# Kernel tuning notes

Measured on AMD Instinct MI355X. Metric: run time of the kernel, lower is better.

The kernel has to match this reference:

```python
import jax, jax.numpy as jnp
import numpy as np

B, S, D, H = 2, 2048, 2048, 16
HD = D // H  # 128
ROPE_BASE = 10000.0


def _rope_tables(seq_len, head_dim, dtype=jnp.float32):
    inv_freq = 1.0 / (ROPE_BASE ** (jnp.arange(0, head_dim, 2, dtype=jnp.float32) / head_dim))
    t = jnp.arange(seq_len, dtype=jnp.float32)
    freqs = jnp.outer(t, inv_freq)  # [S, HD/2]
    # broadcast shape [1, S, 1, HD/2]
    return jnp.cos(freqs)[None, :, None, :].astype(dtype), jnp.sin(freqs)[None, :, None, :].astype(dtype)


def _apply_rope(x, cos, sin):
    # x: [B, S, H, HD]; interleaved split, output concatenated by halves (matches torch code)
    x1 = x[..., ::2]
    x2 = x[..., 1::2]
    return jnp.concatenate([x1 * cos - x2 * sin, x1 * sin + x2 * cos], axis=-1)


def setup_inputs() -> dict:
    key = jax.random.key(0)
    ks = jax.random.split(key, 9)
    xavier = lambda k: jax.random.uniform(k, (D, D), jnp.float32, -1.0, 1.0) * np.sqrt(6.0 / (D + D))
    return {
        "x": jax.random.normal(ks[0], (B, S, D), jnp.float32),
        "attention_mask": jnp.ones((B, S), jnp.int32),
        "wq": xavier(ks[1]), "bq": jnp.zeros((D,), jnp.float32),
        "wk": xavier(ks[2]), "bk": jnp.zeros((D,), jnp.float32),
        "wv": xavier(ks[3]), "bv": jnp.zeros((D,), jnp.float32),
        "wo": xavier(ks[4]), "bo": jnp.zeros((D,), jnp.float32),
    }


def reference(x, attention_mask, wq, bq, wk, bk, wv, bv, wo, bo):
    b, s, _ = x.shape
    scale = HD ** -0.5
    q = (x @ wq + bq).reshape(b, s, H, HD)
    k = (x @ wk + bk).reshape(b, s, H, HD)
    v = (x @ wv + bv).reshape(b, s, H, HD)
    cos, sin = _rope_tables(s, HD, x.dtype)
    q = _apply_rope(q, cos, sin)
    k = _apply_rope(k, cos, sin)
    # [B, H, S, S]
    scores = jnp.einsum('bqhd,bkhd->bhqk', q, k) * scale
    mask = attention_mask[:, None, None, :]  # 2D mask -> [B,1,1,S]
    scores = jnp.where(mask == 0, jnp.asarray(-1e9, scores.dtype), scores)
    attn = jax.nn.softmax(scores, axis=-1)
    out = jnp.einsum('bhqk,bkhd->bqhd', attn, v).reshape(b, s, D)
    return out @ wo + bo
```

## Files before the change

kernel.cpp:

```cpp
#include <hip/hip_runtime.h>

#define Bc 2
#define Sc 2048
#define Dc 2048
#define Hc 16
#define HDc 128
#define Mc 4096

typedef __bf16 bf16_t;
typedef __bf16 bf16x4 __attribute__((ext_vector_type(4)));
typedef __bf16 bf16x8 __attribute__((ext_vector_type(8)));
typedef float f32x4 __attribute__((ext_vector_type(4)));
typedef float f32x16 __attribute__((ext_vector_type(16)));

__device__ __forceinline__ f32x4 mfma16(bf16x8 a, bf16x8 b, f32x4 c) {
  return __builtin_amdgcn_mfma_f32_16x16x32_bf16(a, b, c, 0, 0, 0);
}
__device__ __forceinline__ f32x16 mfma32(bf16x8 a, bf16x8 b, f32x16 c) {
  return __builtin_amdgcn_mfma_f32_32x32x16_bf16(a, b, c, 0, 0, 0);
}

typedef const unsigned __attribute__((address_space(1))) gu32_t;
typedef unsigned __attribute__((address_space(3))) lu32_t;

__device__ __forceinline__ void gload_lds16(const void* g, void* l) {
  gu32_t* gp = (gu32_t*)(unsigned long long)g;
  lu32_t* lp = (lu32_t*)(unsigned)(unsigned long long)l;
  __builtin_amdgcn_global_load_lds(gp, lp, 16, 0, 0);
}

__device__ __forceinline__ unsigned cvtpk(float lo, float hi_) {
  unsigned r;
  asm("v_cvt_pk_bf16_f32 %0, %1, %2" : "=v"(r) : "v"(lo), "v"(hi_));
  return r;
}
__device__ __forceinline__ void plswap(unsigned& a, unsigned& b) {
  asm volatile("v_permlane32_swap_b32 %0, %1" : "+v"(a), "+v"(b));
}

__global__ void cvt_bf16_kernel(const float* __restrict__ in, bf16_t* __restrict__ out, int n4) {
  int i = blockIdx.x * blockDim.x + threadIdx.x;
  if (i < n4) {
    float4 v = ((const float4*)in)[i];
    bf16x4 o;
    o[0] = (bf16_t)v.x; o[1] = (bf16_t)v.y; o[2] = (bf16_t)v.z; o[3] = (bf16_t)v.w;
    ((bf16x4*)out)[i] = o;
  }
}

__global__ void transpose_cvt_kernel(const float* __restrict__ w, bf16_t* __restrict__ wt) {
  __shared__ float tile[32][33];
  const int tx = threadIdx.x, ty = threadIdx.y;
  const int n0 = blockIdx.x * 32, k0 = blockIdx.y * 32;
#pragma unroll
  for (int i = 0; i < 32; i += 8)
    tile[ty + i][tx] = w[(size_t)(k0 + ty + i) * Dc + n0 + tx];
  __syncthreads();
#pragma unroll
  for (int i = 0; i < 32; i += 8)
    wt[(size_t)(n0 + ty + i) * Dc + k0 + tx] = (bf16_t)tile[tx][ty + i];
}

template <int MODE, int NT>
__global__ __launch_bounds__(512, 1) void gemm3_kernel(
    const bf16_t* __restrict__ A, const bf16_t* __restrict__ Bt,
    const float* __restrict__ bias0, const float* __restrict__ bias1,
    const float* __restrict__ bias2,
    void* __restrict__ out0, void* __restrict__ out1, void* __restrict__ out2) {
  __shared__ __align__(16) bf16_t sA[3][128 * 64];
  __shared__ __align__(16) bf16_t sB[3][256 * 64];
  const int tid = threadIdx.x;
  const int lane = tid & 63, wid = tid >> 6;
  const int l15 = lane & 15, g = lane >> 4;
  const int sw = l15 & 7;
  const int wrow = wid >> 2, wcol = wid & 3;

  const int nwg = 32 * NT, cpx = nwg / 8;
  const int wgid = ((int)blockIdx.x & 7) * cpx + ((int)blockIdx.x >> 3);
  const int mt = wgid & 31, nt = wgid >> 5;
  const int m0 = mt * 128, n0 = nt * 256;

  const bf16_t* Ab = A + (size_t)m0 * 2048;
  const bf16_t* Bb = Bt + (size_t)n0 * 2048;

#define G3_STAGE(kt)                                                          \
  {                                                                           \
    const int sl_ = (kt) % 3;                                                 \
    const int kc_ = (kt) * 64;                                                \
    _Pragma("unroll") for (int i_ = 0; i_ < 2; ++i_) {                        \
      int s_ = i_ * 512 + tid;                                                \
      int r_ = s_ >> 3;                                                       \
      int c_ = ((s_ & 7) ^ (r_ & 7)) * 8;                                     \
      gload_lds16(Ab + (size_t)r_ * 2048 + kc_ + c_,                          \
                  (char*)&sA[sl_][0] + s_ * 16);                              \
    }                                                                         \
    _Pragma("unroll") for (int i_ = 0; i_ < 4; ++i_) {                        \
      int s_ = i_ * 512 + tid;                                                \
      int r_ = s_ >> 3;                                                       \
      int c_ = ((s_ & 7) ^ (r_ & 7)) * 8;                                     \
      gload_lds16(Bb + (size_t)r_ * 2048 + kc_ + c_,                          \
                  (char*)&sB[sl_][0] + s_ * 16);                              \
    }                                                                         \
  }

  f32x4 acc[4][4] = {};

  G3_STAGE(0);
  G3_STAGE(1);

#define G3_RD(co)                                                                   \
  _Pragma("unroll") for (int mi = 0; mi < 4; ++mi)                                  \
      afrag[mi] = *(const bf16x8*)(pA + (wrow * 64 + mi * 16 + l15) * 128 + (co));  \
  _Pragma("unroll") for (int ni = 0; ni < 4; ++ni)                                  \
      bfrag[ni] = *(const bf16x8*)(pB + (wcol * 64 + ni * 16 + l15) * 128 + (co));

#define G3_MM                                                                 \
  __builtin_amdgcn_s_setprio(1);                                              \
  _Pragma("unroll") for (int mi = 0; mi < 4; ++mi)                            \
      _Pragma("unroll") for (int ni = 0; ni < 4; ++ni)                        \
          acc[mi][ni] = mfma16(afrag[mi], bfrag[ni], acc[mi][ni]);            \
  __builtin_amdgcn_s_setprio(0);

#define G3_BODY(t, DOSTG, VMSTR)                                              \
  {                                                                           \
    asm volatile("s_waitcnt vmcnt(" VMSTR ")" ::: "memory");                  \
    __builtin_amdgcn_s_barrier();                                             \
    __builtin_amdgcn_sched_barrier(0);                                        \
    const int sl = (t) % 3;                                                   \
    const char* pA = (const char*)&sA[sl][0];                                 \
    const char* pB = (const char*)&sB[sl][0];                                 \
    bf16x8 afrag[4], bfrag[4];                                                \
    G3_RD((g ^ sw) * 16);                                                     \
    if (DOSTG) G3_STAGE((t) + 2);                                             \
    G3_MM;                                                                    \
    G3_RD(((4 + g) ^ sw) * 16);                                               \
    G3_MM;                                                                    \
  }

  for (int t = 0; t < 30; ++t) G3_BODY(t, 1, "6");
  G3_BODY(30, 0, "6");
  G3_BODY(31, 0, "0");

#undef G3_BODY
#undef G3_MM
#undef G3_RD
#undef G3_STAGE

#pragma unroll
  for (int mi = 0; mi < 4; ++mi) {
#pragma unroll
    for (int ni = 0; ni < 4; ++ni) {
      const int ncol = n0 + wcol * 64 + ni * 16 + l15;
      if (MODE == 2) {
        const float bv = bias0[ncol];
#pragma unroll
        for (int r = 0; r < 4; ++r) {
          const int mrow = m0 + wrow * 64 + mi * 16 + g * 4 + r;
          ((float*)out0)[(size_t)mrow * 2048 + ncol] = acc[mi][ni][r] + bv;
        }
      } else {
        const int proj = ncol >> 11, nloc = ncol & 2047;
        const float* bp = proj == 0 ? bias0 : (proj == 1 ? bias1 : bias2);
        bf16_t* op = (bf16_t*)(proj == 0 ? out0 : (proj == 1 ? out1 : out2));
        const float bv = bp[nloc];
        const int h = nloc >> 7, hd = nloc & 127;
#pragma unroll
        for (int r = 0; r < 4; ++r) {
          const int mrow = m0 + wrow * 64 + mi * 16 + g * 4 + r;
          const int b = mrow >> 11, sq = mrow & 2047;
          const float v = acc[mi][ni][r] + bv;
          if (proj < 2)
            op[(((size_t)(b * Hc + h) * Sc + sq) * HDc) + hd] = (bf16_t)v;
          else
            op[(((size_t)(b * Hc + h) * HDc + hd) * Sc) + sq] = (bf16_t)v;
        }
      }
    }
  }
}

__global__ __launch_bounds__(256) void rope_kernel(bf16_t* __restrict__ qk) {
  const int w = threadIdx.x >> 6, lane = threadIdx.x & 63;
  const long row = (long)blockIdx.x * 4 + w;
  const int s = (int)(row & (Sc - 1));
  bf16_t* p = qk + row * HDc;
  float x1 = (float)p[2 * lane];
  float x2 = (float)p[2 * lane + 1];
  float freq = expf(-(float)lane * (9.210340371976184f / 64.0f));
  float ang = (float)s * freq;
  float sn, cs;
  sincosf(ang, &sn, &cs);
  __syncthreads();
  p[lane] = (bf16_t)(x1 * cs - x2 * sn);
  p[lane + 64] = (bf16_t)(x1 * sn + x2 * cs);
}

__global__ __launch_bounds__(256, 2) void attn_kernel(
    const bf16_t* __restrict__ Q, const bf16_t* __restrict__ Kr,
    const bf16_t* __restrict__ Vt, const int* __restrict__ mask,
    bf16_t* __restrict__ AO) {
  __shared__ __align__(16) bf16_t sK[2][64 * 128];
  __shared__ __align__(16) bf16_t sV[2][64 * 128];
  __shared__ float mbias[Sc];
  __shared__ float bcast[4][32];
  const int tid = threadIdx.x;
  const int w = tid >> 6, lane = tid & 63;
  const int l31 = lane & 31, hi = lane >> 5;
  const int wbase = w * 64;

  const int bid = blockIdx.x;
  const int L = ((bid & 7) << 6) + (bid >> 3);
  const int qc = L & 15, h = (L >> 4) & 15, b = L >> 8;

  const int* mb = mask + b * Sc;
#pragma unroll
  for (int i = 0; i < Sc / 256; ++i)
    mbias[i * 256 + tid] = mb[i * 256 + tid] ? 0.f : -1e9f;

  const int q0 = qc * 128 + w * 32;
  const bf16_t* qb = Q + ((size_t)(b * Hc + h) * Sc + q0) * HDc;
  const bf16_t* kb = Kr + ((size_t)(b * Hc + h) * Sc) * HDc;
  const bf16_t* vb = Vt + ((size_t)(b * Hc + h) * HDc) * Sc;

  bf16x8 qf[8];
  {
    const bf16_t* qr = qb + (size_t)l31 * HDc + hi * 8;
#pragma unroll
    for (int kk = 0; kk < 8; ++kk) qf[kk] = *(const bf16x8*)(qr + kk * 16);
  }

#define STAGE_KV(sKb, sVb, kv0_)                                             \
  {                                                                          \
    _Pragma("unroll") for (int p = 0; p < 4; ++p) {                          \
      int s_ = p * 256 + tid;                                                \
      int rk = s_ >> 4, ck = s_ & 15;                                        \
      gload_lds16(kb + (size_t)((kv0_) + rk) * HDc + ((ck ^ (rk & 15)) * 8), \
                  (char*)(sKb) + (size_t)(p * 256 + wbase) * 16);            \
      int d63 = s_ >> 4, sv = s_ & 15;                                       \
      int tmp = sv ^ (d63 & 15);                                             \
      int hb = tmp >> 3, cv = tmp & 7;                                       \
      gload_lds16(vb + (size_t)(hb * 64 + d63) * Sc + (kv0_) + cv * 8,       \
                  (char*)(sVb) + (size_t)(p * 256 + wbase) * 16);            \
    }                                                                        \
  }

  bf16_t* sKc = &sK[0][0];
  bf16_t* sKn = &sK[1][0];
  bf16_t* sVc = &sV[0][0];
  bf16_t* sVn = &sV[1][0];

  STAGE_KV(sKc, sVc, 0);
  asm volatile("s_waitcnt vmcnt(0)" ::: "memory");
  __syncthreads();

  f32x16 acc[4];
#pragma unroll
  for (int d = 0; d < 4; ++d) acc[d] = 0.f;
  float mrun = -3.0e38f, lrun = 0.f;
  const float scale = 0.08838834764831845f;

  for (int kv0 = 0; kv0 < Sc; kv0 += 64) {
    if (kv0 + 64 < Sc) STAGE_KV(sKn, sVn, kv0 + 64);

    f32x16 s0 = 0.f, s1 = 0.f;
    {
      const char* kbase = (const char*)sKc;
      __builtin_amdgcn_s_setprio(1);
#pragma unroll
      for (int kk = 0; kk < 8; ++kk) {
        bf16x8 k0f = *(const bf16x8*)(kbase + l31 * 256 + (((2 * kk + hi) ^ (l31 & 15)) * 16));
        bf16x8 k1f = *(const bf16x8*)(kbase + (32 + l31) * 256 + (((2 * kk + hi) ^ ((32 + l31) & 15)) * 16));
        s0 = mfma32(k0f, qf[kk], s0);
        s1 = mfma32(k1f, qf[kk], s1);
      }
      __builtin_amdgcn_s_setprio(0);
    }
    float v[32];
    {
      const float* mp = mbias + kv0 + 4 * hi;
#pragma unroll
      for (int g4 = 0; g4 < 4; ++g4) {
        f32x4 b0 = *(const f32x4*)(mp + 8 * g4);
        f32x4 b1 = *(const f32x4*)(mp + 32 + 8 * g4);
#pragma unroll
        for (int j = 0; j < 4; ++j) {
          v[g4 * 4 + j] = s0[g4 * 4 + j] * scale + b0[j];
          v[16 + g4 * 4 + j] = s1[g4 * 4 + j] * scale + b1[j];
        }
      }
    }
    float tm = v[0];
#pragma unroll
    for (int r = 1; r < 32; ++r) tm = fmaxf(tm, v[r]);
    tm = fmaxf(tm, __shfl_xor(tm, 32));
    if (__any(tm > mrun + 8.f)) {
      float mnew = fmaxf(mrun, tm);
      float al = __expf(mrun - mnew);
      mrun = mnew;
      lrun *= al;
      bcast[w][l31] = al;
      asm volatile("s_waitcnt lgkmcnt(0)" ::: "memory");
      __builtin_amdgcn_sched_barrier(0);
#pragma unroll
      for (int g4 = 0; g4 < 4; ++g4) {
        f32x4 alr = *(const f32x4*)(&bcast[w][8 * g4 + 4 * hi]);
#pragma unroll
        for (int dblk = 0; dblk < 4; ++dblk)
#pragma unroll
          for (int j = 0; j < 4; ++j) acc[dblk][g4 * 4 + j] *= alr[j];
      }
    }
    float ts = 0.f;
#pragma unroll
    for (int r = 0; r < 32; ++r) {
      v[r] = __expf(v[r] - mrun);
      ts += v[r];
    }
    ts += __shfl_xor(ts, 32);
    lrun += ts;
    unsigned pk[4][4];
#pragma unroll
    for (int ks = 0; ks < 4; ++ks) {
      unsigned a1 = cvtpk(v[ks * 8 + 0], v[ks * 8 + 1]);
      unsigned b1 = cvtpk(v[ks * 8 + 4], v[ks * 8 + 5]);
      unsigned a2 = cvtpk(v[ks * 8 + 2], v[ks * 8 + 3]);
      unsigned b2 = cvtpk(v[ks * 8 + 6], v[ks * 8 + 7]);
      plswap(a1, b1);
      plswap(a2, b2);
      pk[ks][0] = a1; pk[ks][1] = a2; pk[ks][2] = b1; pk[ks][3] = b2;
    }
    {
      const char* vbase = (const char*)sVc;
      __builtin_amdgcn_s_setprio(1);
#pragma unroll
      for (int ks = 0; ks < 4; ++ks) {
        bf16x8 pa = *(const bf16x8*)&pk[ks][0];
#pragma unroll
        for (int dblk = 0; dblk < 4; ++dblk) {
          int d = dblk * 32 + l31;
          int slot = (((d >> 6) * 8 + (2 * ks + hi)) ^ (d & 15));
          bf16x8 vf = *(const bf16x8*)(vbase + (d & 63) * 256 + slot * 16);
          acc[dblk] = mfma32(pa, vf, acc[dblk]);
        }
      }
      __builtin_amdgcn_s_setprio(0);
    }
    asm volatile("s_waitcnt vmcnt(0)" ::: "memory");
    __syncthreads();
    bf16_t* t1 = sKc; sKc = sKn; sKn = t1;
    bf16_t* t2 = sVc; sVc = sVn; sVn = t2;
  }

  float inv = 1.f / lrun;
  bcast[w][l31] = inv;
  asm volatile("s_waitcnt lgkmcnt(0)" ::: "memory");
  __builtin_amdgcn_sched_barrier(0);
  bf16_t* ob = AO + ((size_t)b * Sc + q0) * Dc + h * HDc;
#pragma unroll
  for (int g4 = 0; g4 < 4; ++g4) {
    f32x4 ir = *(const f32x4*)(&bcast[w][8 * g4 + 4 * hi]);
#pragma unroll
    for (int j = 0; j < 4; ++j) {
      int q = 8 * g4 + 4 * hi + j;
#pragma unroll
      for (int dblk = 0; dblk < 4; ++dblk)
        ob[(size_t)q * Dc + dblk * 32 + l31] = (bf16_t)(acc[dblk][g4 * 4 + j] * ir[j]);
    }
  }
}

#define MB(x) ((size_t)(x) << 20)

extern "C" void kernel_launch(void* const* d_in, const int* in_sizes, int n_in,
                              void* d_out, int out_size, void* d_ws, size_t ws_size,
                              hipStream_t stream) {
  const float* x = (const float*)d_in[0];
  const int* mask = (const int*)d_in[1];
  const float* wq = (const float*)d_in[2];
  const float* bq = (const float*)d_in[3];
  const float* wk = (const float*)d_in[4];
  const float* bk = (const float*)d_in[5];
  const float* wv = (const float*)d_in[6];
  const float* bv = (const float*)d_in[7];
  const float* wo = (const float*)d_in[8];
  const float* bo = (const float*)d_in[9];
  float* out = (float*)d_out;

  char* ws = (char*)d_ws;
  bf16_t* xb     = (bf16_t*)(ws + MB(0));
  bf16_t* wqkvT  = (bf16_t*)(ws + MB(16));
  bf16_t* woT    = (bf16_t*)(ws + MB(40));
  bf16_t* qbuf   = (bf16_t*)(ws + MB(48));
  bf16_t* kbuf   = (bf16_t*)(ws + MB(64));
  bf16_t* vtb    = (bf16_t*)(ws + MB(80));
  bf16_t* ao     = (bf16_t*)(ws + MB(96));

  cvt_bf16_kernel<<<8192, 256, 0, stream>>>(x, xb, (Mc * Dc) / 4);

  dim3 tg(64, 64), tb(32, 8);
  transpose_cvt_kernel<<<tg, tb, 0, stream>>>(wq, wqkvT);
  transpose_cvt_kernel<<<tg, tb, 0, stream>>>(wk, wqkvT + (size_t)Dc * Dc);
  transpose_cvt_kernel<<<tg, tb, 0, stream>>>(wv, wqkvT + 2 * (size_t)Dc * Dc);
  transpose_cvt_kernel<<<tg, tb, 0, stream>>>(wo, woT);

  gemm3_kernel<0, 24><<<768, 512, 0, stream>>>(xb, wqkvT, bq, bk, bv, qbuf, kbuf, vtb);

  rope_kernel<<<(2 * Bc * Hc * Sc) / 4, 256, 0, stream>>>(qbuf);

  attn_kernel<<<Bc * Hc * (Sc / 128), 256, 0, stream>>>(qbuf, kbuf, vtb, mask, ao);

  gemm3_kernel<2, 8><<<256, 512, 0, stream>>>(ao, woT, bo, bo, bo, out, out, out);
}
```

Measured before the change: 311.3 us.

## Swap GEMM tile to 256x128 and split k-step into two barrier-separated halves

Replaces the 128x256 GEMM tile with a 256x128 tile and moves the waves from a 2x4 to a 4x2 layout. Each k-step now reads A fragments plus the first half of the B fragments, issues half of the next stage's global-to-LDS loads, and runs the MFMAs. It then hits a second barrier, reads the remaining B fragments, issues the rest of the loads and finishes the MFMAs. The aim is to interleave memory issue with matrix work more finely and to change how LDS reads and tiles map to the hardware. The extra barrier per k-step adds synchronisation cost.

```diff
diff --git a/kernel.cpp b/kernel.cpp
--- a/kernel.cpp
+++ b/kernel.cpp
@@ -61,90 +61,99 @@
     wt[(size_t)(n0 + ty + i) * Dc + k0 + tx] = (bf16_t)tile[tx][ty + i];
 }
 
-template <int MODE, int NT>
-__global__ __launch_bounds__(512, 1) void gemm3_kernel(
+template <int MODE, int NT8>
+__global__ __launch_bounds__(512, 1) void gemmp_kernel(
     const bf16_t* __restrict__ A, const bf16_t* __restrict__ Bt,
     const float* __restrict__ bias0, const float* __restrict__ bias1,
     const float* __restrict__ bias2,
     void* __restrict__ out0, void* __restrict__ out1, void* __restrict__ out2) {
-  __shared__ __align__(16) bf16_t sA[3][128 * 64];
-  __shared__ __align__(16) bf16_t sB[3][256 * 64];
+  __shared__ __align__(16) bf16_t sA[3][256 * 64];
+  __shared__ __align__(16) bf16_t sB[3][128 * 64];
   const int tid = threadIdx.x;
   const int lane = tid & 63, wid = tid >> 6;
   const int l15 = lane & 15, g = lane >> 4;
-  const int sw = l15 & 7;
-  const int wrow = wid >> 2, wcol = wid & 3;
-
-  const int nwg = 32 * NT, cpx = nwg / 8;
+  const int wrow = wid >> 1, wcol = wid & 1;
+
+  const int nwg = 16 * NT8, cpx = nwg / 8;
   const int wgid = ((int)blockIdx.x & 7) * cpx + ((int)blockIdx.x >> 3);
-  const int mt = wgid & 31, nt = wgid >> 5;
-  const int m0 = mt * 128, n0 = nt * 256;
+  const int nt = wgid % NT8, mt = wgid / NT8;
+  const int m0 = mt * 256, n0 = nt * 128;
 
   const bf16_t* Ab = A + (size_t)m0 * 2048;
   const bf16_t* Bb = Bt + (size_t)n0 * 2048;
 
-#define G3_STAGE(kt)                                                          \
-  {                                                                           \
-    const int sl_ = (kt) % 3;                                                 \
-    const int kc_ = (kt) * 64;                                                \
-    _Pragma("unroll") for (int i_ = 0; i_ < 2; ++i_) {                        \
-      int s_ = i_ * 512 + tid;                                                \
-      int r_ = s_ >> 3;                                                       \
-      int c_ = ((s_ & 7) ^ (r_ & 7)) * 8;                                     \
-      gload_lds16(Ab + (size_t)r_ * 2048 + kc_ + c_,                          \
-                  (char*)&sA[sl_][0] + s_ * 16);                              \
-    }                                                                         \
-    _Pragma("unroll") for (int i_ = 0; i_ < 4; ++i_) {                        \
-      int s_ = i_ * 512 + tid;                                                \
-      int r_ = s_ >> 3;                                                       \
-      int c_ = ((s_ & 7) ^ (r_ & 7)) * 8;                                     \
-      gload_lds16(Bb + (size_t)r_ * 2048 + kc_ + c_,                          \
-                  (char*)&sB[sl_][0] + s_ * 16);                              \
-    }                                                                         \
+#define GP_STAGE_A(kt, i_)                                           \
+  {                                                                  \
+    int s_ = (i_) * 512 + tid;                                       \
+    int r_ = s_ >> 3;                                                \
+    int c_ = ((s_ & 7) ^ (r_ & 7)) * 8;                              \
+    gload_lds16(Ab + (size_t)r_ * 2048 + (kt) * 64 + c_,             \
+                (char*)&sA[(kt) % 3][0] + s_ * 16);                  \
+  }
+#define GP_STAGE_B(kt, i_)                                           \
+  {                                                                  \
+    int s_ = (i_) * 512 + tid;                                       \
+    int r_ = s_ >> 3;                                                \
+    int c_ = ((s_ & 7) ^ (r_ & 7)) * 8;                              \
+    gload_lds16(Bb + (size_t)r_ * 2048 + (kt) * 64 + c_,             \
+                (char*)&sB[(kt) % 3][0] + s_ * 16);                  \
   }
 
   f32x4 acc[4][4] = {};
 
-  G3_STAGE(0);
-  G3_STAGE(1);
-
-#define G3_RD(co)                                                                   \
-  _Pragma("unroll") for (int mi = 0; mi < 4; ++mi)                                  \
-      afrag[mi] = *(const bf16x8*)(pA + (wrow * 64 + mi * 16 + l15) * 128 + (co));  \
-  _Pragma("unroll") for (int ni = 0; ni < 4; ++ni)                                  \
-      bfrag[ni] = *(const bf16x8*)(pB + (wcol * 64 + ni * 16 + l15) * 128 + (co));
-
-#define G3_MM                                                                 \
-  __builtin_amdgcn_s_setprio(1);                                              \
-  _Pragma("unroll") for (int mi = 0; mi < 4; ++mi)                            \
-      _Pragma("unroll") for (int ni = 0; ni < 4; ++ni)                        \
-          acc[mi][ni] = mfma16(afrag[mi], bfrag[ni], acc[mi][ni]);            \
-  __builtin_amdgcn_s_setprio(0);
-
-#define G3_BODY(t, DOSTG, VMSTR)                                              \
-  {                                                                           \
-    asm volatile("s_waitcnt vmcnt(" VMSTR ")" ::: "memory");                  \
-    __builtin_amdgcn_s_barrier();                                             \
-    __builtin_amdgcn_sched_barrier(0);                                        \
-    const int sl = (t) % 3;                                                   \
-    const char* pA = (const char*)&sA[sl][0];                                 \
-    const char* pB = (const char*)&sB[sl][0];                                 \
-    bf16x8 afrag[4], bfrag[4];                                                \
-    G3_RD((g ^ sw) * 16);                                                     \
-    if (DOSTG) G3_STAGE((t) + 2);                                             \
-    G3_MM;                                                                    \
-    G3_RD(((4 + g) ^ sw) * 16);                                               \
-    G3_MM;                                                                    \
-  }
-
-  for (int t = 0; t < 30; ++t) G3_BODY(t, 1, "6");
-  G3_BODY(30, 0, "6");
-  G3_BODY(31, 0, "0");
-
-#undef G3_BODY
-#undef G3_MM
-#undef G3_RD
-#undef G3_STAGE
+  GP_STAGE_A(0, 0) GP_STAGE_A(0, 1) GP_STAGE_A(0, 2) GP_STAGE_A(0, 3)
+  GP_STAGE_B(0, 0) GP_STAGE_B(0, 1)
+  GP_STAGE_A(1, 0) GP_STAGE_A(1, 1) GP_STAGE_A(1, 2) GP_STAGE_A(1, 3)
+  GP_STAGE_B(1, 0) GP_STAGE_B(1, 1)
+
+#define GP_BODY(t, DOSTG, VMSTR)                                               \
+  {                                                                            \
+    asm volatile("s_waitcnt vmcnt(" VMSTR ")" ::: "memory");                   \
+    __builtin_amdgcn_s_barrier();       \
+    __builtin_amdgcn_sched_barrier(0);                                         \
+    const char* pA = (const char*)&sA[(t) % 3][0];                             \
+    const char* pB = (const char*)&sB[(t) % 3][0];                             \
+    bf16x8 af[4][2], bf0[2][2], bf1[2][2];                                     \
+    _Pragma("unroll") for (int mi = 0; mi < 4; ++mi)                           \
+        _Pragma("unroll") for (int ks = 0; ks < 2; ++ks) {                     \
+      int r = wrow * 64 + mi * 16 + l15;                                       \
+      af[mi][ks] = *(const bf16x8*)(pA + r * 128 + (((ks * 4 + g) ^ (r & 7)) * 16)); \
+    }                                                                          \
+    _Pragma("unroll") for (int ni = 0; ni < 2; ++ni)                           \
+        _Pragma("unroll") for (int ks = 0; ks < 2; ++ks) {                     \
+      int r = wcol * 64 + ni * 16 + l15;                                       \
+      bf0[ni][ks] = *(const bf16x8*)(pB + r * 128 + (((ks * 4 + g) ^ (r & 7)) * 16)); \
+    }                                                                          \
+    if (DOSTG) { GP_STAGE_A((t) + 2, 0) GP_STAGE_A((t) + 2, 1) GP_STAGE_B((t) + 2, 0) } \
+    __builtin_amdgcn_s_setprio(1);                                             \
+    _Pragma("unroll") for (int mi = 0; mi < 4; ++mi)                           \
+        _Pragma("unroll") for (int ni = 0; ni < 2; ++ni)                       \
+            _Pragma("unroll") for (int ks = 0; ks < 2; ++ks)                   \
+                acc[mi][ni] = mfma16(af[mi][ks], bf0[ni][ks], acc[mi][ni]);    \
+    __builtin_amdgcn_s_setprio(0);                                             \
+    __builtin_amdgcn_s_barrier();                           \
+    __builtin_amdgcn_sched_barrier(0);                                         \
+    _Pragma("unroll") for (int ni = 0; ni < 2; ++ni)                           \
+        _Pragma("unroll") for (int ks = 0; ks < 2; ++ks) {                     \
+      int r = wcol * 64 + (ni + 2) * 16 + l15;                                 \
+      bf1[ni][ks] = *(const bf16x8*)(pB + r * 128 + (((ks * 4 + g) ^ (r & 7)) * 16)); \
+    }                                                                          \
+    if (DOSTG) { GP_STAGE_A((t) + 2, 2) GP_STAGE_A((t) + 2, 3) GP_STAGE_B((t) + 2, 1) } \
+    __builtin_amdgcn_s_setprio(1);                                             \
+    _Pragma("unroll") for (int mi = 0; mi < 4; ++mi)                           \
+        _Pragma("unroll") for (int ni = 0; ni < 2; ++ni)                       \
+            _Pragma("unroll") for (int ks = 0; ks < 2; ++ks)                   \
+                acc[mi][ni + 2] = mfma16(af[mi][ks], bf1[ni][ks], acc[mi][ni + 2]); \
+    __builtin_amdgcn_s_setprio(0);                                             \
+  }
+
+  for (int t = 0; t < 30; ++t) GP_BODY(t, 1, "6");
+  GP_BODY(30, 0, "6");
+  GP_BODY(31, 0, "0");
+
+#undef GP_BODY
+#undef GP_STAGE_A
+#undef GP_STAGE_B
 
 #pragma unroll
   for (int mi = 0; mi < 4; ++mi) {
@@ -403,11 +412,11 @@
   transpose_cvt_kernel<<<tg, tb, 0, stream>>>(wv, wqkvT + 2 * (size_t)Dc * Dc);
   transpose_cvt_kernel<<<tg, tb, 0, stream>>>(wo, woT);
 
-  gemm3_kernel<0, 24><<<768, 512, 0, stream>>>(xb, wqkvT, bq, bk, bv, qbuf, kbuf, vtb);
+  gemmp_kernel<0, 48><<<768, 512, 0, stream>>>(xb, wqkvT, bq, bk, bv, qbuf, kbuf, vtb);
 
   rope_kernel<<<(2 * Bc * Hc * Sc) / 4, 256, 0, stream>>>(qbuf);
 
   attn_kernel<<<Bc * Hc * (Sc / 128), 256, 0, stream>>>(qbuf, kbuf, vtb, mask, ao);
 
-  gemm3_kernel<2, 8><<<256, 512, 0, stream>>>(ao, woT, bo, bo, bo, out, out, out);
-}
+  gemmp_kernel<2, 16><<<256, 512, 0, stream>>>(ao, woT, bo, bo, bo, out, out, out);
+}
```

Result: faster. 299.9 us (-3.7%).

## Enlarge GEMM tile to 256x256 with K=32 stages and paired-row LDS swizzle

Applied to the files above, without the earlier changes.

The GEMM kernel now computes 256x256 output tiles instead of 128x256. Each stage covers K=32, and the LDS layout packs two rows per 128-byte line with an XOR swizzle. Each wave now holds 8x4 MFMA accumulators, which raises operand reuse and halves the number of workgroups, so less global and LDS traffic is needed per FLOP. The cost is higher register pressure. The QKV projection launches 384 blocks and the output projection only 128, which leaves many of the 256 CUs idle in the output GEMM.

```diff
diff --git a/kernel.cpp b/kernel.cpp
--- a/kernel.cpp
+++ b/kernel.cpp
@@ -62,92 +62,87 @@
 }
 
 template <int MODE, int NT>
-__global__ __launch_bounds__(512, 1) void gemm3_kernel(
+__global__ __launch_bounds__(512, 1) void gemmx_kernel(
     const bf16_t* __restrict__ A, const bf16_t* __restrict__ Bt,
     const float* __restrict__ bias0, const float* __restrict__ bias1,
     const float* __restrict__ bias2,
     void* __restrict__ out0, void* __restrict__ out1, void* __restrict__ out2) {
-  __shared__ __align__(16) bf16_t sA[3][128 * 64];
-  __shared__ __align__(16) bf16_t sB[3][256 * 64];
+  __shared__ __align__(16) bf16_t sA[3][256 * 32];
+  __shared__ __align__(16) bf16_t sB[3][256 * 32];
   const int tid = threadIdx.x;
   const int lane = tid & 63, wid = tid >> 6;
   const int l15 = lane & 15, g = lane >> 4;
-  const int sw = l15 & 7;
   const int wrow = wid >> 2, wcol = wid & 3;
 
-  const int nwg = 32 * NT, cpx = nwg / 8;
+  const int nwg = 16 * NT, cpx = nwg / 8;
   const int wgid = ((int)blockIdx.x & 7) * cpx + ((int)blockIdx.x >> 3);
-  const int mt = wgid & 31, nt = wgid >> 5;
-  const int m0 = mt * 128, n0 = nt * 256;
+  const int nt = wgid % NT, mt = wgid / NT;
+  const int m0 = mt * 256, n0 = nt * 256;
 
   const bf16_t* Ab = A + (size_t)m0 * 2048;
   const bf16_t* Bb = Bt + (size_t)n0 * 2048;
 
-#define G3_STAGE(kt)                                                          \
-  {                                                                           \
-    const int sl_ = (kt) % 3;                                                 \
-    const int kc_ = (kt) * 64;                                                \
-    _Pragma("unroll") for (int i_ = 0; i_ < 2; ++i_) {                        \
-      int s_ = i_ * 512 + tid;                                                \
-      int r_ = s_ >> 3;                                                       \
-      int c_ = ((s_ & 7) ^ (r_ & 7)) * 8;                                     \
-      gload_lds16(Ab + (size_t)r_ * 2048 + kc_ + c_,                          \
-                  (char*)&sA[sl_][0] + s_ * 16);                              \
-    }                                                                         \
-    _Pragma("unroll") for (int i_ = 0; i_ < 4; ++i_) {                        \
-      int s_ = i_ * 512 + tid;                                                \
-      int r_ = s_ >> 3;                                                       \
-      int c_ = ((s_ & 7) ^ (r_ & 7)) * 8;                                     \
-      gload_lds16(Bb + (size_t)r_ * 2048 + kc_ + c_,                          \
-                  (char*)&sB[sl_][0] + s_ * 16);                              \
-    }                                                                         \
-  }
-
-  f32x4 acc[4][4] = {};
-
-  G3_STAGE(0);
-  G3_STAGE(1);
-
-#define G3_RD(co)                                                                   \
-  _Pragma("unroll") for (int mi = 0; mi < 4; ++mi)                                  \
-      afrag[mi] = *(const bf16x8*)(pA + (wrow * 64 + mi * 16 + l15) * 128 + (co));  \
-  _Pragma("unroll") for (int ni = 0; ni < 4; ++ni)                                  \
-      bfrag[ni] = *(const bf16x8*)(pB + (wcol * 64 + ni * 16 + l15) * 128 + (co));
-
-#define G3_MM                                                                 \
-  __builtin_amdgcn_s_setprio(1);                                              \
-  _Pragma("unroll") for (int mi = 0; mi < 4; ++mi)                            \
-      _Pragma("unroll") for (int ni = 0; ni < 4; ++ni)                        \
-          acc[mi][ni] = mfma16(afrag[mi], bfrag[ni], acc[mi][ni]);            \
-  __builtin_amdgcn_s_setprio(0);
-
-#define G3_BODY(t, DOSTG, VMSTR)                                              \
-  {                                                                           \
-    asm volatile("s_waitcnt vmcnt(" VMSTR ")" ::: "memory");                  \
-    __builtin_amdgcn_s_barrier();                                             \
-    __builtin_amdgcn_sched_barrier(0);                                        \
-    const int sl = (t) % 3;                                                   \
-    const char* pA = (const char*)&sA[sl][0];                                 \
-    const char* pB = (const char*)&sB[sl][0];                                 \
-    bf16x8 afrag[4], bfrag[4];                                                \
-    G3_RD((g ^ sw) * 16);                                                     \
-    if (DOSTG) G3_STAGE((t) + 2);                                             \
-    G3_MM;                                                                    \
-    G3_RD(((4 + g) ^ sw) * 16);                                               \
-    G3_MM;                                                                    \
-  }
-
-  for (int t = 0; t < 30; ++t) G3_BODY(t, 1, "6");
-  G3_BODY(30, 0, "6");
-  G3_BODY(31, 0, "0");
-
-#undef G3_BODY
-#undef G3_MM
-#undef G3_RD
-#undef G3_STAGE
-
-#pragma unroll
-  for (int mi = 0; mi < 4; ++mi) {
+#define GX_STAGE(kt)                                                  \
+  {                                                                   \
+    const int sl_ = (kt) % 3;                                         \
+    _Pragma("unroll") for (int i_ = 0; i_ < 2; ++i_) {                \
+      int s_ = i_ * 512 + tid;                                        \
+      int rp_ = s_ >> 3, cs_ = (s_ & 7) ^ (rp_ & 7);                  \
+      int sr_ = 2 * rp_ + (cs_ >> 2);                                 \
+      int sk_ = (kt) * 32 + (cs_ & 3) * 8;                            \
+      gload_lds16(Ab + (size_t)sr_ * 2048 + sk_,                      \
+                  (char*)&sA[sl_][0] + s_ * 16);                      \
+    }                                                                 \
+    _Pragma("unroll") for (int i_ = 0; i_ < 2; ++i_) {                \
+      int s_ = i_ * 512 + tid;                                        \
+      int rp_ = s_ >> 3, cs_ = (s_ & 7) ^ (rp_ & 7);                  \
+      int sr_ = 2 * rp_ + (cs_ >> 2);                                 \
+      int sk_ = (kt) * 32 + (cs_ & 3) * 8;                            \
+      gload_lds16(Bb + (size_t)sr_ * 2048 + sk_,                      \
+                  (char*)&sB[sl_][0] + s_ * 16);                      \
+    }                                                                 \
+  }
+
+  f32x4 acc[8][4] = {};
+
+  GX_STAGE(0);
+  GX_STAGE(1);
+
+#define GX_BODY(t, DOSTG, VMSTR)                                             \
+  {                                                                          \
+    asm volatile("s_waitcnt vmcnt(" VMSTR ")" ::: "memory");                 \
+    __builtin_amdgcn_s_barrier(); \
+    __builtin_amdgcn_sched_barrier(0);                                       \
+    const char* pA = (const char*)&sA[(t) % 3][0];                           \
+    const char* pB = (const char*)&sB[(t) % 3][0];                           \
+    bf16x8 af[8], bfr[4];                                                    \
+    _Pragma("unroll") for (int mi = 0; mi < 8; ++mi) {                       \
+      int ra = wrow * 128 + mi * 16 + l15;                                   \
+      int rp = ra >> 1, cs = (ra & 1) * 4 + g;                               \
+      af[mi] = *(const bf16x8*)(pA + rp * 128 + ((cs ^ (rp & 7)) * 16));     \
+    }                                                                        \
+    _Pragma("unroll") for (int ni = 0; ni < 4; ++ni) {                       \
+      int rb = wcol * 64 + ni * 16 + l15;                                    \
+      int rp = rb >> 1, cs = (rb & 1) * 4 + g;                               \
+      bfr[ni] = *(const bf16x8*)(pB + rp * 128 + ((cs ^ (rp & 7)) * 16));    \
+    }                                                                        \
+    if (DOSTG) GX_STAGE((t) + 2);                                            \
+    __builtin_amdgcn_s_setprio(1);                                           \
+    _Pragma("unroll") for (int mi = 0; mi < 8; ++mi)                         \
+      _Pragma("unroll") for (int ni = 0; ni < 4; ++ni)                       \
+          acc[mi][ni] = mfma16(af[mi], bfr[ni], acc[mi][ni]);                \
+    __builtin_amdgcn_s_setprio(0);                                           \
+  }
+
+  for (int t = 0; t < 62; ++t) GX_BODY(t, 1, "4");
+  GX_BODY(62, 0, "4");
+  GX_BODY(63, 0, "0");
+
+#undef GX_BODY
+#undef GX_STAGE
+
+#pragma unroll
+  for (int mi = 0; mi < 8; ++mi) {
 #pragma unroll
     for (int ni = 0; ni < 4; ++ni) {
       const int ncol = n0 + wcol * 64 + ni * 16 + l15;
@@ -155,7 +150,7 @@
         const float bv = bias0[ncol];
 #pragma unroll
         for (int r = 0; r < 4; ++r) {
-          const int mrow = m0 + wrow * 64 + mi * 16 + g * 4 + r;
+          const int mrow = m0 + wrow * 128 + mi * 16 + g * 4 + r;
           ((float*)out0)[(size_t)mrow * 2048 + ncol] = acc[mi][ni][r] + bv;
         }
       } else {
@@ -166,7 +161,7 @@
         const int h = nloc >> 7, hd = nloc & 127;
 #pragma unroll
         for (int r = 0; r < 4; ++r) {
-          const int mrow = m0 + wrow * 64 + mi * 16 + g * 4 + r;
+          const int mrow = m0 + wrow * 128 + mi * 16 + g * 4 + r;
           const int b = mrow >> 11, sq = mrow & 2047;
           const float v = acc[mi][ni][r] + bv;
           if (proj < 2)
@@ -403,11 +398,11 @@
   transpose_cvt_kernel<<<tg, tb, 0, stream>>>(wv, wqkvT + 2 * (size_t)Dc * Dc);
   transpose_cvt_kernel<<<tg, tb, 0, stream>>>(wo, woT);
 
-  gemm3_kernel<0, 24><<<768, 512, 0, stream>>>(xb, wqkvT, bq, bk, bv, qbuf, kbuf, vtb);
+  gemmx_kernel<0, 24><<<384, 512, 0, stream>>>(xb, wqkvT, bq, bk, bv, qbuf, kbuf, vtb);
 
   rope_kernel<<<(2 * Bc * Hc * Sc) / 4, 256, 0, stream>>>(qbuf);
 
   attn_kernel<<<Bc * Hc * (Sc / 128), 256, 0, stream>>>(qbuf, kbuf, vtb, mask, ao);
 
-  gemm3_kernel<2, 8><<<256, 512, 0, stream>>>(ao, woT, bo, bo, bo, out, out, out);
-}
+  gemmx_kernel<2, 8><<<128, 512, 0, stream>>>(ao, woT, bo, bo, bo, out, out, out);
+}
```

Result: slower. 326.8 us (+5.0%).
